# Kernel tuning notes

Hardware: AMD Instinct MI355X
Metric: run time of the kernel (lower is better)

## Reference

```python
import jax, jax.numpy as jnp
import numpy as np

B, T, C, H = 2, 2048, 1024, 16
D = C // H  # head dim


def setup_inputs() -> dict:
    key = jax.random.key(0)
    ks = jax.random.split(key, 10)
    s = 1.0 / np.sqrt(C)  # xavier-ish scale
    inp = {
        "q": jax.random.normal(ks[0], (B, T, C), jnp.float32),
        "k": jax.random.normal(ks[1], (B, T, C), jnp.float32),
        "Wq": jax.random.normal(ks[2], (C, C), jnp.float32) * s,
        "bq": jnp.zeros((C,), jnp.float32),
        "Wk": jax.random.normal(ks[3], (C, C), jnp.float32) * s,
        "bk": jnp.zeros((C,), jnp.float32),
        "Wv": jax.random.normal(ks[4], (C, C), jnp.float32) * s,
        "bv": jnp.zeros((C,), jnp.float32),
        "Wo": jax.random.normal(ks[5], (C, C), jnp.float32) * s,
        "bo": jnp.zeros((C,), jnp.float32),
        # causal mask (lower triangular); masked_fill where mask == 0
        "mask": jnp.tril(jnp.ones((T, T), jnp.int32))[None, None],
    }
    return inp


def reference(q, k, Wq, bq, Wk, bk, Wv, bv, Wo, bo, mask):
    # projections (weights stored input-major: y = x @ W + b)
    qp = q @ Wq + bq                       # [B,T,C]
    kp = k @ Wk + bk                       # [B,T,C]
    vp = kp @ Wv + bv                      # quirk: V computed from projected K

    def heads(x):
        return x.reshape(B, T, H, D).transpose(0, 2, 1, 3)  # [B,H,T,D]

    qh, kh, vh = heads(qp), heads(kp), heads(vp)
    scores = jnp.einsum("bhqd,bhkd->bhqk", qh, kh) / jnp.sqrt(jnp.float32(D))
    scores = jnp.where(mask == 0, -jnp.inf, scores)
    attention_weights = jax.nn.softmax(scores, axis=-1)  # [B,H,T,T]
    # dropout omitted (eval mode / p=0)
    ctx = jnp.einsum("bhqk,bhkd->bhqd", attention_weights, vh)
    ctx = ctx.transpose(0, 2, 1, 3).reshape(B, T, C)
    out = ctx @ Wo + bo
    return out, attention_weights
```

## Files before the change

kernel.cpp:

```cpp
#include <hip/hip_runtime.h>

typedef __attribute__((ext_vector_type(8))) short bf16x8;
typedef __attribute__((ext_vector_type(4))) float f32x4;
typedef unsigned short u16;
typedef unsigned int u32;

#define T_SEQ 2048
#define C_DIM 1024
#define NH 16
#define HD 64
#define BATCH 2

__device__ __forceinline__ u16 f2bf(float f) {
    union { float f; u32 u; } v; v.f = f;
    u32 u = v.u;
    u32 r = (u + 0x7FFFu + ((u >> 16) & 1u)) >> 16;
    return (u16)r;
}

__device__ __forceinline__ float fexp2(float x) { return __builtin_amdgcn_exp2f(x); }

__device__ __forceinline__ void gld_lds16(const void* g, void* l) {
    __builtin_amdgcn_global_load_lds(
        (const __attribute__((address_space(1))) void*)g,
        (__attribute__((address_space(3))) void*)l, 16, 0, 0);
}

__global__ __launch_bounds__(256) void transpose_to_bf16(
    const float* __restrict__ W0, const float* __restrict__ W1,
    const float* __restrict__ W2, const float* __restrict__ W3,
    u16* __restrict__ O0, u16* __restrict__ O1,
    u16* __restrict__ O2, u16* __restrict__ O3)
{
    __shared__ float tile[32][33];
    const float* W = blockIdx.z == 0 ? W0 : blockIdx.z == 1 ? W1 : blockIdx.z == 2 ? W2 : W3;
    u16* O = blockIdx.z == 0 ? O0 : blockIdx.z == 1 ? O1 : blockIdx.z == 2 ? O2 : O3;
    const int tx = threadIdx.x, ty = threadIdx.y;
    const int bx = blockIdx.x * 32, by = blockIdx.y * 32;
#pragma unroll
    for (int i = 0; i < 4; ++i)
        tile[ty + i * 8][tx] = W[(size_t)(by + ty + i * 8) * C_DIM + bx + tx];
    __syncthreads();
#pragma unroll
    for (int i = 0; i < 4; ++i)
        O[(size_t)(bx + ty + i * 8) * C_DIM + by + tx] = f2bf(tile[tx][ty + i * 8]);
}

template<bool XF32, int OMODE>
__global__ __launch_bounds__(256) void gemm_bt(
    const void* __restrict__ X0_, const void* __restrict__ X1_,
    const u16* __restrict__ W0T, const u16* __restrict__ W1T,
    const float* __restrict__ b0_, const float* __restrict__ b1_,
    void* __restrict__ Y0_, void* __restrict__ Y1_,
    int M, int N, int K)
{
    __shared__ u16 As[64 * 32];
    __shared__ u16 Bs[128 * 32];
    const int tid = threadIdx.x;
    const int w = tid >> 6, l = tid & 63;
    const int lr = l & 15, lg = l >> 4;
    const int z = blockIdx.z;
    const void* Xv = z ? X1_ : X0_;
    const u16* WT = z ? W1T : W0T;
    const float* bias = z ? b1_ : b0_;
    void* Yv = z ? Y1_ : Y0_;
    const int m0 = blockIdx.y * 64, n0 = blockIdx.x * 128;
    const int grow = l >> 2, gcol = (l & 3) * 8;
    f32x4 acc[4][2] = {};

    for (int k0 = 0; k0 < K; k0 += 32) {
        __syncthreads();
        if (XF32) {
            const int row = tid >> 2, cg = tid & 3;
            const float* g = (const float*)Xv + (size_t)(m0 + row) * K + k0 + cg * 8;
            float4 a0 = *(const float4*)g;
            float4 a1 = *(const float4*)(g + 4);
            union { u16 h[8]; uint4 q; } pk;
            pk.h[0] = f2bf(a0.x); pk.h[1] = f2bf(a0.y);
            pk.h[2] = f2bf(a0.z); pk.h[3] = f2bf(a0.w);
            pk.h[4] = f2bf(a1.x); pk.h[5] = f2bf(a1.y);
            pk.h[6] = f2bf(a1.z); pk.h[7] = f2bf(a1.w);
            *(uint4*)&As[row * 32 + cg * 8] = pk.q;
        } else {
            gld_lds16((const u16*)Xv + (size_t)(m0 + w * 16 + grow) * K + k0 + gcol,
                      &As[w * 512]);
        }
#pragma unroll
        for (int i = 0; i < 2; ++i)
            gld_lds16(WT + (size_t)(n0 + w * 32 + i * 16 + grow) * K + k0 + gcol,
                      &Bs[(w * 2 + i) * 512]);
        __syncthreads();
        bf16x8 af[4], bfr[2];
#pragma unroll
        for (int i = 0; i < 4; ++i)
            af[i] = *(const bf16x8*)&As[(i * 16 + lr) * 32 + lg * 8];
#pragma unroll
        for (int j = 0; j < 2; ++j)
            bfr[j] = *(const bf16x8*)&Bs[(w * 32 + j * 16 + lr) * 32 + lg * 8];
#pragma unroll
        for (int i = 0; i < 4; ++i)
#pragma unroll
            for (int j = 0; j < 2; ++j)
                acc[i][j] = __builtin_amdgcn_mfma_f32_16x16x32_bf16(af[i], bfr[j], acc[i][j], 0, 0, 0);
    }

#pragma unroll
    for (int i = 0; i < 4; ++i) {
        const int rowb = m0 + i * 16 + lg * 4;
#pragma unroll
        for (int j = 0; j < 2; ++j) {
            const int col = n0 + w * 32 + j * 16 + lr;
            const float bv = bias[col];
            if (OMODE == 2) {
                union { u16 h[4]; uint2 q; } pk;
#pragma unroll
                for (int r = 0; r < 4; ++r) pk.h[r] = f2bf(acc[i][j][r] + bv);
                const int bb = rowb >> 11, tt = rowb & 2047;
                const int hh = col >> 6, dd = col & 63;
                u16* dst = (u16*)Yv + ((size_t)((bb * NH + hh) * HD + dd)) * T_SEQ + tt;
                *(uint2*)dst = pk.q;
            } else {
#pragma unroll
                for (int r = 0; r < 4; ++r) {
                    const float v = acc[i][j][r] + bv;
                    if (OMODE == 1)
                        ((float*)Yv)[(size_t)(rowb + r) * N + col] = v;
                    else
                        ((u16*)Yv)[(size_t)(rowb + r) * N + col] = f2bf(v);
                }
            }
        }
    }
}

#define PV_QS 67
#define PV_WS (16 * PV_QS + 8)

__global__ __launch_bounds__(1024) void attn_kernel(
    const u16* __restrict__ qp, const u16* __restrict__ kp,
    const u16* __restrict__ vt, u16* __restrict__ ctx,
    float* __restrict__ attn)
{
    __shared__ float statm[16][16], statl[16][16];
    __shared__ float pvbuf[16 * PV_WS];

    const int tid = threadIdx.x;
    const int w = tid >> 6, l = tid & 63;
    const int lr = l & 15, lg = l >> 4;

    const int wgid = (blockIdx.x & 7) * 512 + (blockIdx.x >> 3);
    const int b = wgid >> 11;
    const int h = (wgid >> 7) & 15;
    const int strip = 127 - (wgid & 127);
    const int q0 = strip * 16;

    const size_t bh_off = (size_t)b * T_SEQ * C_DIM + h * HD;
    const u16* qb = qp + bh_off;
    const u16* kb = kp + bh_off;
    const u16* vtb = vt + ((size_t)(b * NH + h) * HD) * T_SEQ;
    float* ab = attn + (size_t)(b * NH + h) * T_SEQ * T_SEQ;

    const float SC = 0.125f * 1.44269504088896f;
    const float MNEG = -1e30f;

    const bf16x8 aq0 = *(const bf16x8*)(qb + (size_t)(q0 + lr) * C_DIM + lg * 8);
    const bf16x8 aq1 = *(const bf16x8*)(qb + (size_t)(q0 + lr) * C_DIM + 32 + lg * 8);

    const int qrow = q0 + lr;
    const int n32 = (q0 + 47) >> 5;

    f32x4 ec[4][2];
    float ml = MNEG;
#pragma unroll
    for (int j = 0; j < 4; ++j) {
        const int ti = w + 16 * j;
        if (ti < n32) {
            const int kvb = ti * 32;
            const u16* kr0 = kb + (size_t)(kvb + lr) * C_DIM;
            const u16* kr1 = kb + (size_t)(kvb + 16 + lr) * C_DIM;
            const bf16x8 k00 = *(const bf16x8*)(kr0 + lg * 8);
            const bf16x8 k01 = *(const bf16x8*)(kr0 + 32 + lg * 8);
            const bf16x8 k10 = *(const bf16x8*)(kr1 + lg * 8);
            const bf16x8 k11 = *(const bf16x8*)(kr1 + 32 + lg * 8);
            f32x4 s[2] = {};
            s[0] = __builtin_amdgcn_mfma_f32_16x16x32_bf16(k00, aq0, s[0], 0, 0, 0);
            s[0] = __builtin_amdgcn_mfma_f32_16x16x32_bf16(k01, aq1, s[0], 0, 0, 0);
            s[1] = __builtin_amdgcn_mfma_f32_16x16x32_bf16(k10, aq0, s[1], 0, 0, 0);
            s[1] = __builtin_amdgcn_mfma_f32_16x16x32_bf16(k11, aq1, s[1], 0, 0, 0);
#pragma unroll
            for (int t = 0; t < 2; ++t)
#pragma unroll
                for (int r = 0; r < 4; ++r) {
                    float v = s[t][r] * SC;
                    if (kvb + 16 * t + 4 * lg + r > qrow) v = MNEG;
                    ec[j][t][r] = v;
                    ml = fmaxf(ml, v);
                }
        } else {
#pragma unroll
            for (int t = 0; t < 2; ++t)
#pragma unroll
                for (int r = 0; r < 4; ++r) ec[j][t][r] = MNEG;
        }
    }
    ml = fmaxf(ml, __shfl_xor(ml, 16));
    ml = fmaxf(ml, __shfl_xor(ml, 32));
    float ll = 0.f;
#pragma unroll
    for (int j = 0; j < 4; ++j)
#pragma unroll
        for (int t = 0; t < 2; ++t)
#pragma unroll
            for (int r = 0; r < 4; ++r) {
                const float e = fexp2(ec[j][t][r] - ml);
                ec[j][t][r] = e;
                ll += e;
            }
    ll += __shfl_xor(ll, 16);
    ll += __shfl_xor(ll, 32);
    if (l < 16) { statm[w][lr] = ml; statl[w][lr] = ll; }
    __syncthreads();

    float mf = MNEG;
#pragma unroll
    for (int ww = 0; ww < 16; ++ww) mf = fmaxf(mf, statm[ww][lr]);
    float lf = 0.f;
#pragma unroll
    for (int ww = 0; ww < 16; ++ww) lf += statl[ww][lr] * fexp2(statm[ww][lr] - mf);
    const float scale = fexp2(ml - mf) / lf;

    f32x4 cacc[4] = {};
#pragma unroll
    for (int j = 0; j < 4; ++j) {
        const int ti = w + 16 * j;
        if (ti < n32) {
            const int kvb = ti * 32;
            bf16x8 vf[4];
#pragma unroll
            for (int dt = 0; dt < 4; ++dt)
                vf[dt] = *(const bf16x8*)(vtb + (size_t)(dt * 16 + lr) * T_SEQ + kvb + lg * 8);
            u32 pw[2][2];
#pragma unroll
            for (int t2 = 0; t2 < 2; ++t2) {
                float p[4];
#pragma unroll
                for (int r = 0; r < 4; ++r) p[r] = ec[j][t2][r] * scale;
                f32x4 pv4 = { p[0], p[1], p[2], p[3] };
                __builtin_nontemporal_store(pv4,
                    (f32x4*)(ab + (size_t)qrow * T_SEQ + kvb + 16 * t2 + 4 * lg));
                pw[t2][0] = (u32)f2bf(p[0]) | ((u32)f2bf(p[1]) << 16);
                pw[t2][1] = (u32)f2bf(p[2]) | ((u32)f2bf(p[3]) << 16);
            }
            const int bl = lr + ((lg & 1) << 5);
            const u32 a0 = (u32)__shfl((int)pw[0][0], bl);
            const u32 a1 = (u32)__shfl((int)pw[0][1], bl);
            const u32 a2 = (u32)__shfl((int)pw[0][0], bl + 16);
            const u32 a3 = (u32)__shfl((int)pw[0][1], bl + 16);
            const u32 b0 = (u32)__shfl((int)pw[1][0], bl);
            const u32 b1 = (u32)__shfl((int)pw[1][1], bl);
            const u32 b2 = (u32)__shfl((int)pw[1][0], bl + 16);
            const u32 b3 = (u32)__shfl((int)pw[1][1], bl + 16);
            const bool hi2 = lg >= 2;
            union { u32 ww[4]; bf16x8 v; } pa;
            pa.ww[0] = hi2 ? b0 : a0;
            pa.ww[1] = hi2 ? b1 : a1;
            pa.ww[2] = hi2 ? b2 : a2;
            pa.ww[3] = hi2 ? b3 : a3;
            __builtin_amdgcn_s_setprio(1);
#pragma unroll
            for (int dt = 0; dt < 4; ++dt)
                cacc[dt] = __builtin_amdgcn_mfma_f32_16x16x32_bf16(pa.v, vf[dt], cacc[dt], 0, 0, 0);
            __builtin_amdgcn_s_setprio(0);
        }
    }

    {
        float* pwv = pvbuf + w * PV_WS;
#pragma unroll
        for (int dt = 0; dt < 4; ++dt)
#pragma unroll
            for (int r = 0; r < 4; ++r)
                pwv[(4 * lg + r) * PV_QS + dt * 16 + lr] = cacc[dt][r];
    }
    __syncthreads();

    {
        const int qq = tid >> 6;
        const int d0 = tid & 63;
        float s0 = 0.f;
#pragma unroll
        for (int ww = 0; ww < 16; ++ww)
            s0 += pvbuf[ww * PV_WS + qq * PV_QS + d0];
        u16* cb = ctx + bh_off;
        cb[(size_t)(q0 + qq) * C_DIM + d0] = f2bf(s0);
    }

    {
        const int zs = n32 * 32;
        const int row = tid >> 6;
        const int c0 = (tid & 63) * 4;
        float* zr = ab + (size_t)(q0 + row) * T_SEQ;
        const f32x4 z4 = { 0.f, 0.f, 0.f, 0.f };
        for (int c = zs + c0; c < T_SEQ; c += 256)
            __builtin_nontemporal_store(z4, (f32x4*)(zr + c));
    }
}

extern "C" void kernel_launch(void* const* d_in, const int* in_sizes, int n_in,
                              void* d_out, int out_size, void* d_ws, size_t ws_size,
                              hipStream_t stream)
{
    const float* q  = (const float*)d_in[0];
    const float* k  = (const float*)d_in[1];
    const float* Wq = (const float*)d_in[2];
    const float* bq = (const float*)d_in[3];
    const float* Wk = (const float*)d_in[4];
    const float* bk = (const float*)d_in[5];
    const float* Wv = (const float*)d_in[6];
    const float* bv = (const float*)d_in[7];
    const float* Wo = (const float*)d_in[8];
    const float* bo = (const float*)d_in[9];
    (void)in_sizes; (void)n_in; (void)out_size; (void)ws_size;

    float* out = (float*)d_out;
    float* attn = out + (size_t)BATCH * T_SEQ * C_DIM;

    const size_t MC = (size_t)BATCH * T_SEQ * C_DIM;
    u16* qp  = (u16*)d_ws;
    u16* kp  = qp + MC;
    u16* vt  = kp + MC;
    u16* ctx = vt + MC;
    u16* WqT = ctx + MC;
    u16* WkT = WqT + (size_t)C_DIM * C_DIM;
    u16* WvT = WkT + (size_t)C_DIM * C_DIM;
    u16* WoT = WvT + (size_t)C_DIM * C_DIM;

    transpose_to_bf16<<<dim3(32, 32, 4), dim3(32, 8), 0, stream>>>(
        Wq, Wk, Wv, Wo, WqT, WkT, WvT, WoT);

    const int M = BATCH * T_SEQ;
    dim3 gqk(C_DIM / 128, M / 64, 2);
    dim3 g1(C_DIM / 128, M / 64, 1);
    gemm_bt<true, 0><<<gqk, 256, 0, stream>>>(q, k, WqT, WkT, bq, bk,
                                              qp, kp, M, C_DIM, C_DIM);
    gemm_bt<false, 2><<<g1, 256, 0, stream>>>(kp, kp, WvT, WvT, bv, bv,
                                              vt, vt, M, C_DIM, C_DIM);

    attn_kernel<<<dim3(4096), 1024, 0, stream>>>(qp, kp, vt, ctx, attn);

    gemm_bt<false, 1><<<g1, 256, 0, stream>>>(ctx, ctx, WoT, WoT, bo, bo,
                                              out, out, M, C_DIM, C_DIM);
}
```

Measured before the change: 287.9 us.

## Halve attention block to 8 waves with per-tile softmax stats stored as bf16

The attention kernel now runs 512 threads (8 waves) per block instead of 1024, so each wave handles up to 8 key tiles. To fit the extra tiles in registers, exponentials are computed per tile against a local max and kept packed as bf16, then rescaled by the per-tile max and global normalizer in the PV pass. The zero-fill of the masked upper triangle moves to the start of the kernel so those stores overlap compute, and the ctx reduction writes two bf16 values per thread. Keeping the probabilities in bf16 before writing the fp32 attention weights lowers their precision, and each wave now carries more serial work.

New measurement: 254.2 us. -11.7%, faster.

```diff
diff --git a/kernel.cpp b/kernel.cpp
--- a/kernel.cpp
+++ b/kernel.cpp
@@ -19,6 +19,13 @@
 }
 
 __device__ __forceinline__ float fexp2(float x) { return __builtin_amdgcn_exp2f(x); }
+
+__device__ __forceinline__ float bflo(u32 u) {
+    union { u32 u; float f; } v; v.u = u << 16; return v.f;
+}
+__device__ __forceinline__ float bfhi(u32 u) {
+    union { u32 u; float f; } v; v.u = u & 0xFFFF0000u; return v.f;
+}
 
 __device__ __forceinline__ void gld_lds16(const void* g, void* l) {
     __builtin_amdgcn_global_load_lds(
@@ -136,13 +143,13 @@
 #define PV_QS 67
 #define PV_WS (16 * PV_QS + 8)
 
-__global__ __launch_bounds__(1024) void attn_kernel(
+__global__ __launch_bounds__(512, 4) void attn_kernel(
     const u16* __restrict__ qp, const u16* __restrict__ kp,
     const u16* __restrict__ vt, u16* __restrict__ ctx,
     float* __restrict__ attn)
 {
-    __shared__ float statm[16][16], statl[16][16];
-    __shared__ float pvbuf[16 * PV_WS];
+    __shared__ float statm[8][16], statl[8][16];
+    __shared__ float pvbuf[8 * PV_WS];
 
     const int tid = threadIdx.x;
     const int w = tid >> 6, l = tid & 63;
@@ -163,17 +170,29 @@
     const float SC = 0.125f * 1.44269504088896f;
     const float MNEG = -1e30f;
 
+    const int qrow = q0 + lr;
+    const int n32 = (q0 + 47) >> 5;
+
+    {
+        const int zs = n32 * 32;
+        const int row = tid >> 5;
+        const int c0 = (tid & 31) * 4;
+        float* zr = ab + (size_t)(q0 + row) * T_SEQ;
+        const f32x4 z4 = { 0.f, 0.f, 0.f, 0.f };
+        for (int c = zs + c0; c < T_SEQ; c += 128)
+            __builtin_nontemporal_store(z4, (f32x4*)(zr + c));
+    }
+
     const bf16x8 aq0 = *(const bf16x8*)(qb + (size_t)(q0 + lr) * C_DIM + lg * 8);
     const bf16x8 aq1 = *(const bf16x8*)(qb + (size_t)(q0 + lr) * C_DIM + 32 + lg * 8);
 
-    const int qrow = q0 + lr;
-    const int n32 = (q0 + 47) >> 5;
-
-    f32x4 ec[4][2];
+    u32 ec[8][2];
+    u32 ec2[8][2];
+    float mtj[8], Sj[8];
     float ml = MNEG;
 #pragma unroll
-    for (int j = 0; j < 4; ++j) {
-        const int ti = w + 16 * j;
+    for (int j = 0; j < 8; ++j) {
+        const int ti = w + 8 * j;
         if (ti < n32) {
             const int kvb = ti * 32;
             const u16* kr0 = kb + (size_t)(kvb + lr) * C_DIM;
@@ -187,64 +206,80 @@
             s[0] = __builtin_amdgcn_mfma_f32_16x16x32_bf16(k01, aq1, s[0], 0, 0, 0);
             s[1] = __builtin_amdgcn_mfma_f32_16x16x32_bf16(k10, aq0, s[1], 0, 0, 0);
             s[1] = __builtin_amdgcn_mfma_f32_16x16x32_bf16(k11, aq1, s[1], 0, 0, 0);
+            float sv[2][4];
+            float mt = MNEG;
 #pragma unroll
             for (int t = 0; t < 2; ++t)
 #pragma unroll
                 for (int r = 0; r < 4; ++r) {
                     float v = s[t][r] * SC;
                     if (kvb + 16 * t + 4 * lg + r > qrow) v = MNEG;
-                    ec[j][t][r] = v;
-                    ml = fmaxf(ml, v);
+                    sv[t][r] = v;
+                    mt = fmaxf(mt, v);
                 }
+            mtj[j] = mt;
+            float ss = 0.f;
+            float e[2][4];
+#pragma unroll
+            for (int t = 0; t < 2; ++t)
+#pragma unroll
+                for (int r = 0; r < 4; ++r) {
+                    e[t][r] = fexp2(sv[t][r] - mt);
+                    ss += e[t][r];
+                }
+            Sj[j] = ss;
+#pragma unroll
+            for (int t = 0; t < 2; ++t) {
+                ec[j][t]  = (u32)f2bf(e[t][0]) | ((u32)f2bf(e[t][1]) << 16);
+                ec2[j][t] = (u32)f2bf(e[t][2]) | ((u32)f2bf(e[t][3]) << 16);
+            }
+            ml = fmaxf(ml, mt);
         } else {
-#pragma unroll
-            for (int t = 0; t < 2; ++t)
-#pragma unroll
-                for (int r = 0; r < 4; ++r) ec[j][t][r] = MNEG;
-        }
-    }
-    ml = fmaxf(ml, __shfl_xor(ml, 16));
-    ml = fmaxf(ml, __shfl_xor(ml, 32));
+            mtj[j] = MNEG; Sj[j] = 0.f;
+            ec[j][0] = ec[j][1] = ec2[j][0] = ec2[j][1] = 0;
+        }
+    }
     float ll = 0.f;
 #pragma unroll
-    for (int j = 0; j < 4; ++j)
-#pragma unroll
-        for (int t = 0; t < 2; ++t)
-#pragma unroll
-            for (int r = 0; r < 4; ++r) {
-                const float e = fexp2(ec[j][t][r] - ml);
-                ec[j][t][r] = e;
-                ll += e;
-            }
-    ll += __shfl_xor(ll, 16);
-    ll += __shfl_xor(ll, 32);
+    for (int j = 0; j < 8; ++j) ll += Sj[j] * fexp2(mtj[j] - ml);
+#pragma unroll
+    for (int d = 16; d <= 32; d <<= 1) {
+        const float mo = __shfl_xor(ml, d);
+        const float lo = __shfl_xor(ll, d);
+        const float mn = fmaxf(ml, mo);
+        ll = ll * fexp2(ml - mn) + lo * fexp2(mo - mn);
+        ml = mn;
+    }
     if (l < 16) { statm[w][lr] = ml; statl[w][lr] = ll; }
     __syncthreads();
 
     float mf = MNEG;
 #pragma unroll
-    for (int ww = 0; ww < 16; ++ww) mf = fmaxf(mf, statm[ww][lr]);
+    for (int ww = 0; ww < 8; ++ww) mf = fmaxf(mf, statm[ww][lr]);
     float lf = 0.f;
 #pragma unroll
-    for (int ww = 0; ww < 16; ++ww) lf += statl[ww][lr] * fexp2(statm[ww][lr] - mf);
-    const float scale = fexp2(ml - mf) / lf;
+    for (int ww = 0; ww < 8; ++ww) lf += statl[ww][lr] * fexp2(statm[ww][lr] - mf);
+    const float rlf = 1.f / lf;
 
     f32x4 cacc[4] = {};
 #pragma unroll
-    for (int j = 0; j < 4; ++j) {
-        const int ti = w + 16 * j;
+    for (int j = 0; j < 8; ++j) {
+        const int ti = w + 8 * j;
         if (ti < n32) {
             const int kvb = ti * 32;
             bf16x8 vf[4];
 #pragma unroll
             for (int dt = 0; dt < 4; ++dt)
                 vf[dt] = *(const bf16x8*)(vtb + (size_t)(dt * 16 + lr) * T_SEQ + kvb + lg * 8);
+            const float scale = fexp2(mtj[j] - mf) * rlf;
             u32 pw[2][2];
 #pragma unroll
             for (int t2 = 0; t2 < 2; ++t2) {
                 float p[4];
-#pragma unroll
-                for (int r = 0; r < 4; ++r) p[r] = ec[j][t2][r] * scale;
+                p[0] = bflo(ec[j][t2]) * scale;
+                p[1] = bfhi(ec[j][t2]) * scale;
+                p[2] = bflo(ec2[j][t2]) * scale;
+                p[3] = bfhi(ec2[j][t2]) * scale;
                 f32x4 pv4 = { p[0], p[1], p[2], p[3] };
                 __builtin_nontemporal_store(pv4,
                     (f32x4*)(ab + (size_t)qrow * T_SEQ + kvb + 16 * t2 + 4 * lg));
@@ -285,24 +320,19 @@
     __syncthreads();
 
     {
-        const int qq = tid >> 6;
-        const int d0 = tid & 63;
-        float s0 = 0.f;
-#pragma unroll
-        for (int ww = 0; ww < 16; ++ww)
-            s0 += pvbuf[ww * PV_WS + qq * PV_QS + d0];
+        const int qq = tid >> 5;
+        const int d0 = (tid & 31) * 2;
+        float s0 = 0.f, s1 = 0.f;
+#pragma unroll
+        for (int ww = 0; ww < 8; ++ww) {
+            const float* pwv = pvbuf + ww * PV_WS + qq * PV_QS;
+            s0 += pwv[d0];
+            s1 += pwv[d0 + 1];
+        }
+        union { u16 hh[2]; u32 u; } pk;
+        pk.hh[0] = f2bf(s0); pk.hh[1] = f2bf(s1);
         u16* cb = ctx + bh_off;
-        cb[(size_t)(q0 + qq) * C_DIM + d0] = f2bf(s0);
-    }
-
-    {
-        const int zs = n32 * 32;
-        const int row = tid >> 6;
-        const int c0 = (tid & 63) * 4;
-        float* zr = ab + (size_t)(q0 + row) * T_SEQ;
-        const f32x4 z4 = { 0.f, 0.f, 0.f, 0.f };
-        for (int c = zs + c0; c < T_SEQ; c += 256)
-            __builtin_nontemporal_store(z4, (f32x4*)(zr + c));
+        *(u32*)(cb + (size_t)(q0 + qq) * C_DIM + d0) = pk.u;
     }
 }
 
@@ -346,7 +376,7 @@
     gemm_bt<false, 2><<<g1, 256, 0, stream>>>(kp, kp, WvT, WvT, bv, bv,
                                               vt, vt, M, C_DIM, C_DIM);
 
-    attn_kernel<<<dim3(4096), 1024, 0, stream>>>(qp, kp, vt, ctx, attn);
+    attn_kernel<<<dim3(4096), 512, 0, stream>>>(qp, kp, vt, ctx, attn);
 
     gemm_bt<false, 1><<<g1, 256, 0, stream>>>(ctx, ctx, WoT, WoT, bo, bo,
                                               out, out, M, C_DIM, C_DIM);
```
